# Kernel tuning notes

Hardware: AMD Instinct MI355X
Metric: run time of the kernel (lower is better)

Reference implementation:

```python
import math
import jax, jax.numpy as jnp
import numpy as np


def _sinkhorn_attn(q, n):
    """Log-domain Sinkhorn-Knopp, eps=1, max_iter=1, uniform marginals.
    cost C = -q @ q^T, so M = (-C + u + v)/eps = S + u + v with S = q q^T.
    Returns transport plan pi = exp(S + u_i + v_j).  q: [B, n, d]."""
    S = jnp.einsum('bnd,bmd->bnm', q, q)            # [B, n, n]
    log_marg = -math.log(n)                          # log(1/n)
    u = log_marg - jax.nn.logsumexp(S, axis=-1)      # [B, n] row update
    v = log_marg - jax.nn.logsumexp(S + u[..., :, None], axis=-2)  # [B, n] col update
    return jnp.exp(S + u[..., :, None] + v[..., None, :])


def reference(x, row_embed, col_embed):
    # x: [B, d, H, W]; row_embed/col_embed: [len_embedding, d//2]
    B, d, H, W = x.shape
    # learned positional embedding: [H, W, d] -> [d, H, W]
    x_emb = col_embed[:W]                             # [W, F]
    y_emb = row_embed[:H]                             # [H, F]
    F = x_emb.shape[-1]
    pos = jnp.concatenate([
        jnp.broadcast_to(x_emb[None, :, :], (H, W, F)),
        jnp.broadcast_to(y_emb[:, None, :], (H, W, F)),
    ], axis=-1).transpose(2, 0, 1)                    # [d, H, W]
    x = x + pos[None]

    n = H * W
    xf = x.reshape(B, d, n).transpose(0, 2, 1)        # [B, n, d] = q = k = v (v unscaled)
    inv_sqrtV = 1.0 / math.sqrt(math.sqrt(d))         # d**-0.25 applied to q and k each
    attn = _sinkhorn_attn(xf * inv_sqrtV, n)          # [B, n, n]
    out = jnp.einsum('bnm,bmd->bnd', attn, xf)        # [B, n, d]
    return out.transpose(0, 2, 1).reshape(B, d, H, W)


def setup_inputs() -> dict:
    key = jax.random.key(0)
    k1, k2, k3 = jax.random.split(key, 3)
    B, d, H, W = 32, 512, 32, 32
    len_emb, F = 32, d // 2
    return {
        'x': jax.random.normal(k1, (B, d, H, W), dtype=jnp.float32),
        'row_embed': jax.random.uniform(k2, (len_emb, F), dtype=jnp.float32),
        'col_embed': jax.random.uniform(k3, (len_emb, F), dtype=jnp.float32),
    }
```

## Files before the change

### kernel.cpp

```cpp
#include <hip/hip_runtime.h>
#include <hip/hip_fp16.h>
#include <math.h>

typedef _Float16 f16;
typedef _Float16 f16x8 __attribute__((ext_vector_type(8)));
typedef _Float16 f16x4 __attribute__((ext_vector_type(4)));
typedef float f32x4 __attribute__((ext_vector_type(4)));

namespace {
constexpr int kB = 32, kD = 512, kN = 1024, kF = 256;
constexpr float kScale = 0.04419417382415922f;
constexpr float kLogMarg = -6.931471805599453f;
constexpr float kMarg = 1.f / 1024.f;
constexpr float kPScale = 16384.f;
constexpr float kPInv = 1.f / 16384.f;
}

__device__ __forceinline__ void gload16(const void* g, void* l) {
  __builtin_amdgcn_global_load_lds(
      (const __attribute__((address_space(1))) void*)g,
      (__attribute__((address_space(3))) void*)l, 16, 0, 0);
}

__global__ __launch_bounds__(256) void k_prep(
    const float* __restrict__ x, const float* __restrict__ re,
    const float* __restrict__ ce, f16* __restrict__ xf,
    f16* __restrict__ xfT, int b0) {
  __shared__ f16 T[64][68];
  const int lb = blockIdx.z;
  const int i0 = blockIdx.x * 64, c0 = blockIdx.y * 64;
  const int t = threadIdx.x;
  const int il = (t & 15) * 4;
  const int cl = t >> 4;
  const size_t xbase = ((size_t)(b0 + lb) * kD) * kN;
#pragma unroll
  for (int p = 0; p < 4; p++) {
    const int c = c0 + cl + 16 * p;
    const int i = i0 + il;
    const float4 xv = *(const float4*)(x + xbase + (size_t)c * kN + i);
    float4 pv;
    if (c < kF) {
      pv.x = ce[((i + 0) & 31) * kF + c];
      pv.y = ce[((i + 1) & 31) * kF + c];
      pv.z = ce[((i + 2) & 31) * kF + c];
      pv.w = ce[((i + 3) & 31) * kF + c];
    } else {
      const float r = re[(i >> 5) * kF + (c - kF)];
      pv.x = r; pv.y = r; pv.z = r; pv.w = r;
    }
    const f16 h0 = (f16)(xv.x + pv.x), h1 = (f16)(xv.y + pv.y);
    const f16 h2 = (f16)(xv.z + pv.z), h3 = (f16)(xv.w + pv.w);
    f16* dT = xfT + ((size_t)lb * kD + c) * kN + i;
    *(f16x4*)dT = (f16x4){h0, h1, h2, h3};
    T[cl + 16 * p][il + 0] = h0; T[cl + 16 * p][il + 1] = h1;
    T[cl + 16 * p][il + 2] = h2; T[cl + 16 * p][il + 3] = h3;
  }
  __syncthreads();
#pragma unroll
  for (int p = 0; p < 4; p++) {
    const int ir = cl + 16 * p;
    const int cc = il;
    const f16 h0 = T[cc + 0][ir], h1 = T[cc + 1][ir];
    const f16 h2 = T[cc + 2][ir], h3 = T[cc + 3][ir];
    f16* dF = xf + ((size_t)lb * kN + i0 + ir) * kD + c0 + cc;
    *(f16x4*)dF = (f16x4){h0, h1, h2, h3};
  }
}

__global__ __launch_bounds__(512) void k_gemm_s(
    const f16* __restrict__ xf, f16* __restrict__ S16,
    float* __restrict__ rp) {
  __shared__ char sm[131072];
  const int nwg = (int)(gridDim.x * gridDim.y * gridDim.z);
  const int lin = (int)(blockIdx.x +
                        gridDim.x * (blockIdx.y + gridDim.y * blockIdx.z));
  const int wid = (lin & 7) * (nwg >> 3) + (lin >> 3);
  const int bx = wid & 3, by = (wid >> 2) & 3, bz = wid >> 4;

  const int lb = bz;
  const int i0 = by * 256, j0 = bx * 256;
  const char* base = (const char*)(xf + (size_t)lb * kN * kD);
  const int t = threadIdx.x;
  const int w = t >> 6, lane = t & 63;
  const int wm = w >> 2, wn = w & 3;
  const int m_off = wm * 128, n_off = wn * 64;
  const int quad = lane >> 4, l15 = lane & 15;
  const int swz = (l15 & 7) << 4;

  int srcA[4], srcB[4], ldsw[4];
#pragma unroll
  for (int p = 0; p < 4; p++) {
    const int off = p * 8192 + t * 16;
    const int r = off >> 7;
    const int cb = (off & 127) ^ ((r & 7) << 4);
    srcA[p] = (i0 + r) * (kD * 2) + cb;
    srcB[p] = (j0 + r) * (kD * 2) + cb;
    ldsw[p] = p * 8192 + w * 1024;
  }

  f32x4 acc[8][4];
#pragma unroll
  for (int a = 0; a < 8; a++)
#pragma unroll
    for (int b = 0; b < 4; b++) acc[a][b] = (f32x4){0.f, 0.f, 0.f, 0.f};

#pragma unroll
  for (int p = 0; p < 4; p++) gload16(base + srcA[p], sm + ldsw[p]);
#pragma unroll
  for (int p = 0; p < 4; p++) gload16(base + srcB[p], sm + 32768 + ldsw[p]);
  __syncthreads();

#pragma unroll
  for (int tt = 0; tt < 8; tt++) {
    const int cur = tt & 1, nxt = cur ^ 1;
    if (tt + 1 < 8) {
      const int k0b = (tt + 1) * 128;
#pragma unroll
      for (int p = 0; p < 4; p++)
        gload16(base + srcA[p] + k0b, sm + (nxt << 16) + ldsw[p]);
#pragma unroll
      for (int p = 0; p < 4; p++)
        gload16(base + srcB[p] + k0b, sm + (nxt << 16) + 32768 + ldsw[p]);
    }
    const char* bA = sm + (cur << 16);
    const char* bB = bA + 32768;
#pragma unroll
    for (int kk = 0; kk < 2; kk++) {
      f16x8 af[8], bf[4];
#pragma unroll
      for (int q = 0; q < 8; q++)
        af[q] = *(const f16x8*)(bA + (m_off + 16 * q + l15) * 128 +
                                ((kk * 64 + quad * 16) ^ swz));
#pragma unroll
      for (int q = 0; q < 4; q++)
        bf[q] = *(const f16x8*)(bB + (n_off + 16 * q + l15) * 128 +
                                ((kk * 64 + quad * 16) ^ swz));
#pragma unroll
      for (int qa = 0; qa < 8; qa++)
#pragma unroll
        for (int qb = 0; qb < 4; qb++)
          acc[qa][qb] = __builtin_amdgcn_mfma_f32_16x16x32_f16(
              af[qa], bf[qb], acc[qa][qb], 0, 0, 0);
    }
    __syncthreads();
  }

  f16* Sb = S16 + (size_t)lb * kN * kN;
  const int jt = bx * 4 + wn;
  float* rpb = rp + ((size_t)lb * 16 + jt) * kN + i0 + m_off;
#pragma unroll
  for (int qa = 0; qa < 8; qa++) {
    const int i = i0 + m_off + 16 * qa + quad * 4;
    float rs[4] = {0.f, 0.f, 0.f, 0.f};
#pragma unroll
    for (int qb = 0; qb < 4; qb++) {
      const int j = j0 + n_off + 16 * qb + l15;
#pragma unroll
      for (int r = 0; r < 4; r++) {
        const f16 h = (f16)(acc[qa][qb][r] * kScale);
        Sb[(size_t)(i + r) * kN + j] = h;
        rs[r] += __expf((float)h);
      }
    }
#pragma unroll
    for (int r = 0; r < 4; r++) {
      float s = rs[r];
      s += __shfl_xor(s, 1);
      s += __shfl_xor(s, 2);
      s += __shfl_xor(s, 4);
      s += __shfl_xor(s, 8);
      if (l15 == 0) rpb[16 * qa + 4 * quad + r] = s;
    }
  }
}

__global__ __launch_bounds__(256) void k_u(
    const float* __restrict__ rp, float* __restrict__ u) {
  const int lb = blockIdx.y;
  const int i = blockIdx.x * 256 + threadIdx.x;
  const float* r = rp + (size_t)lb * 16 * kN + i;
  float s = 0.f;
#pragma unroll
  for (int t = 0; t < 16; t++) s += r[(size_t)t * kN];
  u[lb * kN + i] = kLogMarg - __logf(s);
}

__global__ __launch_bounds__(256) void k_cs(
    const f16* __restrict__ S16, const float* __restrict__ u,
    float* __restrict__ cp, f16* __restrict__ E16) {
  const int lb = blockIdx.z;
  const int seg = blockIdx.y;
  const int j = blockIdx.x * 256 + threadIdx.x;
  const f16* Sb = S16 + (size_t)lb * kN * kN + j;
  f16* Eb = E16 + (size_t)lb * kN * kN + j;
  const float* ub = u + lb * kN + seg * 64;
  const size_t rbase = (size_t)(seg * 64) * kN;
  float s = 0.f;
#pragma unroll 4
  for (int r = 0; r < 64; r++) {
    const float eS = __expf((float)Sb[rbase + (size_t)r * kN] + ub[r]);
    s += eS;
    Eb[rbase + (size_t)r * kN] = (f16)(eS * kPScale);
  }
  cp[((size_t)lb * 16 + seg) * kN + j] = s;
}

__global__ __launch_bounds__(256) void k_v(
    const float* __restrict__ cp, float* __restrict__ ev) {
  const int lb = blockIdx.y;
  const int j = blockIdx.x * 256 + threadIdx.x;
  const float* c = cp + (size_t)lb * 16 * kN + j;
  float s = 0.f;
#pragma unroll
  for (int r = 0; r < 16; r++) s += c[(size_t)r * kN];
  ev[lb * kN + j] = kMarg / s;
}

__global__ __launch_bounds__(512) void k_gemm_o(
    const f16* __restrict__ xfT, const f16* __restrict__ E16,
    const float* __restrict__ ev, float* __restrict__ out, int b0) {
  __shared__ char sm[131072];
  const int nwg = (int)(gridDim.x * gridDim.y * gridDim.z);
  const int lin = (int)(blockIdx.x +
                        gridDim.x * (blockIdx.y + gridDim.y * blockIdx.z));
  const int wid = (lin & 7) * (nwg >> 3) + (lin >> 3);
  const int bx = wid & 3, by = (wid >> 2) & 1, bz = wid >> 3;

  const int lb = bz;
  const int i0 = bx * 256, c0 = by * 256;
  const char* Ab = (const char*)(xfT + (size_t)lb * kD * kN);
  const char* Bb = (const char*)(E16 + (size_t)lb * kN * kN);
  const float* evb = ev + (size_t)lb * kN;
  const int t = threadIdx.x;
  const int w = t >> 6, lane = t & 63;
  const int wm = w >> 2, wn = w & 3;
  const int m_off = wm * 128, n_off = wn * 64;
  const int quad = lane >> 4, l15 = lane & 15;
  const int swz = (l15 & 7) << 4;

  int srcAlin[4], dstA[4], srcB[4], ldsw[4], evcol[4];
#pragma unroll
  for (int p = 0; p < 4; p++) {
    const int off = p * 8192 + t * 16;
    const int r = off >> 7;
    const int cbl = off & 127;
    const int cb = cbl ^ ((r & 7) << 4);
    srcAlin[p] = (c0 + r) * (kN * 2) + cbl;
    dstA[p] = r * 128 + cb;
    srcB[p] = (i0 + r) * (kN * 2) + cb;
    ldsw[p] = p * 8192 + w * 1024;
    evcol[p] = cbl >> 1;
  }

  f32x4 acc[8][4];
#pragma unroll
  for (int a = 0; a < 8; a++)
#pragma unroll
    for (int b = 0; b < 4; b++) acc[a][b] = (f32x4){0.f, 0.f, 0.f, 0.f};

  f16x8 al[4];
  float4 e0[4], e1[4];
#pragma unroll
  for (int p = 0; p < 4; p++) {
    al[p] = *(const f16x8*)(Ab + srcAlin[p]);
    e0[p] = *(const float4*)(evb + evcol[p]);
    e1[p] = *(const float4*)(evb + evcol[p] + 4);
  }
#pragma unroll
  for (int p = 0; p < 4; p++) gload16(Bb + srcB[p], sm + 32768 + ldsw[p]);
#pragma unroll
  for (int p = 0; p < 4; p++) {
    f16x8 pr;
    pr[0] = (f16)((float)al[p][0] * e0[p].x);
    pr[1] = (f16)((float)al[p][1] * e0[p].y);
    pr[2] = (f16)((float)al[p][2] * e0[p].z);
    pr[3] = (f16)((float)al[p][3] * e0[p].w);
    pr[4] = (f16)((float)al[p][4] * e1[p].x);
    pr[5] = (f16)((float)al[p][5] * e1[p].y);
    pr[6] = (f16)((float)al[p][6] * e1[p].z);
    pr[7] = (f16)((float)al[p][7] * e1[p].w);
    *(f16x8*)(sm + dstA[p]) = pr;
  }
  __syncthreads();

#pragma unroll
  for (int tt = 0; tt < 16; tt++) {
    const int cur = tt & 1, nxt = cur ^ 1;
    const bool pf = (tt + 1 < 16);
    if (pf) {
      const int k0b = (tt + 1) * 128;
      const int k0f = (tt + 1) * 64;
#pragma unroll
      for (int p = 0; p < 4; p++) {
        al[p] = *(const f16x8*)(Ab + srcAlin[p] + k0b);
        e0[p] = *(const float4*)(evb + k0f + evcol[p]);
        e1[p] = *(const float4*)(evb + k0f + evcol[p] + 4);
      }
#pragma unroll
      for (int p = 0; p < 4; p++)
        gload16(Bb + srcB[p] + k0b, sm + (nxt << 16) + 32768 + ldsw[p]);
    }
    const char* bA = sm + (cur << 16);
    const char* bB = bA + 32768;
#pragma unroll
    for (int kk = 0; kk < 2; kk++) {
      f16x8 af[8], bf[4];
#pragma unroll
      for (int q = 0; q < 8; q++)
        af[q] = *(const f16x8*)(bA + (m_off + 16 * q + l15) * 128 +
                                ((kk * 64 + quad * 16) ^ swz));
#pragma unroll
      for (int q = 0; q < 4; q++)
        bf[q] = *(const f16x8*)(bB + (n_off + 16 * q + l15) * 128 +
                                ((kk * 64 + quad * 16) ^ swz));
#pragma unroll
      for (int qa = 0; qa < 8; qa++)
#pragma unroll
        for (int qb = 0; qb < 4; qb++)
          acc[qa][qb] = __builtin_amdgcn_mfma_f32_16x16x32_f16(
              af[qa], bf[qb], acc[qa][qb], 0, 0, 0);
    }
    if (pf) {
#pragma unroll
      for (int p = 0; p < 4; p++) {
        f16x8 pr;
        pr[0] = (f16)((float)al[p][0] * e0[p].x);
        pr[1] = (f16)((float)al[p][1] * e0[p].y);
        pr[2] = (f16)((float)al[p][2] * e0[p].z);
        pr[3] = (f16)((float)al[p][3] * e0[p].w);
        pr[4] = (f16)((float)al[p][4] * e1[p].x);
        pr[5] = (f16)((float)al[p][5] * e1[p].y);
        pr[6] = (f16)((float)al[p][6] * e1[p].z);
        pr[7] = (f16)((float)al[p][7] * e1[p].w);
        *(f16x8*)(sm + (nxt << 16) + dstA[p]) = pr;
      }
    }
    __syncthreads();
  }

  float* ob = out + ((size_t)(b0 + lb) * kD) * kN;
#pragma unroll
  for (int qa = 0; qa < 8; qa++) {
    const int c = c0 + m_off + 16 * qa + quad * 4;
#pragma unroll
    for (int qb = 0; qb < 4; qb++) {
      const int i = i0 + n_off + 16 * qb + l15;
#pragma unroll
      for (int r = 0; r < 4; r++)
        ob[(size_t)(c + r) * kN + i] = acc[qa][qb][r] * kPInv;
    }
  }
}

extern "C" void kernel_launch(void* const* d_in, const int* in_sizes, int n_in,
                              void* d_out, int out_size, void* d_ws, size_t ws_size,
                              hipStream_t stream) {
  const float* x = (const float*)d_in[0];
  const float* re = (const float*)d_in[1];
  const float* ce = (const float*)d_in[2];
  float* out = (float*)d_out;

  char* wsb = (char*)d_ws;
  const size_t perb = 2097152ull + 1048576 + 1048576 + 2097152 +
                      4096 + 4096 + 65536 + 65536;
  int G = (int)(ws_size / perb);
  if (G >= 32) G = 32;
  else if (G >= 16) G = 16;
  else if (G >= 8) G = 8;
  else if (G >= 4) G = 4;
  else if (G < 1) G = 1;
  f16* S16 = (f16*)wsb;
  f16* xf = (f16*)(wsb + (size_t)G * 2097152);
  f16* xfT = (f16*)((char*)xf + (size_t)G * 1048576);
  f16* E16 = (f16*)((char*)xfT + (size_t)G * 1048576);
  float* u = (float*)((char*)E16 + (size_t)G * 2097152);
  float* ev = u + (size_t)G * kN;
  float* rp = ev + (size_t)G * kN;
  float* cp = rp + (size_t)G * 16 * kN;

  for (int b0 = 0; b0 < kB; b0 += G) {
    const int g = (kB - b0 < G) ? (kB - b0) : G;
    k_prep<<<dim3(16, 8, g), 256, 0, stream>>>(x, re, ce, xf, xfT, b0);
    k_gemm_s<<<dim3(4, 4, g), 512, 0, stream>>>(xf, S16, rp);
    k_u<<<dim3(4, g), 256, 0, stream>>>(rp, u);
    k_cs<<<dim3(4, 16, g), 256, 0, stream>>>(S16, u, cp, E16);
    k_v<<<dim3(4, g), 256, 0, stream>>>(cp, ev);
    k_gemm_o<<<dim3(4, 2, g), 512, 0, stream>>>(xfT, E16, ev, out, b0);
  }
}
```

Baseline: 257.0 us.

## Interleave async LDS loads with MFMA in both GEMMs; prescale V in separate kernel

Both GEMM main loops are restructured so the next tile's global-to-LDS loads are issued in pieces between MFMA groups. Explicit vmcnt waits, raw s_barrier calls and s_setprio replace __syncthreads, and the A fragments are loaded per sub-block to reduce register pressure. The ev column scaling of V, previously done in registers inside k_gemm_o, moves into a new k_va kernel that writes a scaled f16 copy aT, so the output GEMM can use direct async LDS loads for both operands. This costs an extra 1 MB per batch of workspace plus one extra read and write pass over xfT.

```diff
diff --git a/kernel.cpp b/kernel.cpp
--- a/kernel.cpp
+++ b/kernel.cpp
@@ -98,51 +98,69 @@
     ldsw[p] = p * 8192 + w * 1024;
   }
 
+#pragma unroll
+  for (int p = 0; p < 4; p++) gload16(base + srcA[p], sm + ldsw[p]);
+#pragma unroll
+  for (int p = 0; p < 4; p++) gload16(base + srcB[p], sm + 32768 + ldsw[p]);
+
   f32x4 acc[8][4];
 #pragma unroll
   for (int a = 0; a < 8; a++)
 #pragma unroll
     for (int b = 0; b < 4; b++) acc[a][b] = (f32x4){0.f, 0.f, 0.f, 0.f};
-
-#pragma unroll
-  for (int p = 0; p < 4; p++) gload16(base + srcA[p], sm + ldsw[p]);
-#pragma unroll
-  for (int p = 0; p < 4; p++) gload16(base + srcB[p], sm + 32768 + ldsw[p]);
-  __syncthreads();
 
 #pragma unroll
   for (int tt = 0; tt < 8; tt++) {
     const int cur = tt & 1, nxt = cur ^ 1;
-    if (tt + 1 < 8) {
-      const int k0b = (tt + 1) * 128;
-#pragma unroll
-      for (int p = 0; p < 4; p++)
-        gload16(base + srcA[p] + k0b, sm + (nxt << 16) + ldsw[p]);
-#pragma unroll
-      for (int p = 0; p < 4; p++)
-        gload16(base + srcB[p] + k0b, sm + (nxt << 16) + 32768 + ldsw[p]);
-    }
-    const char* bA = sm + (cur << 16);
-    const char* bB = bA + 32768;
-#pragma unroll
-    for (int kk = 0; kk < 2; kk++) {
-      f16x8 af[8], bf[4];
-#pragma unroll
-      for (int q = 0; q < 8; q++)
-        af[q] = *(const f16x8*)(bA + (m_off + 16 * q + l15) * 128 +
-                                ((kk * 64 + quad * 16) ^ swz));
-#pragma unroll
-      for (int q = 0; q < 4; q++)
-        bf[q] = *(const f16x8*)(bB + (n_off + 16 * q + l15) * 128 +
-                                ((kk * 64 + quad * 16) ^ swz));
-#pragma unroll
-      for (int qa = 0; qa < 8; qa++)
+    const char* rA = sm + (cur << 16);
+    const char* rB = rA + 32768;
+    char* wA = sm + (nxt << 16);
+    char* wB = wA + 32768;
+    const int k0b = (tt + 1) * 128;
+    f16x8 bf[4][2];
+#pragma unroll
+    for (int q = 0; q < 4; q++) {
+      if (q == 0) {
+        if (tt + 1 < 8) {
+          gload16(base + srcA[0] + k0b, wA + ldsw[0]);
+          gload16(base + srcB[0] + k0b, wB + ldsw[0]);
+          asm volatile("s_waitcnt vmcnt(2)" ::: "memory");
+        } else {
+          asm volatile("s_waitcnt vmcnt(0)" ::: "memory");
+        }
+        __builtin_amdgcn_s_barrier();
 #pragma unroll
         for (int qb = 0; qb < 4; qb++)
-          acc[qa][qb] = __builtin_amdgcn_mfma_f32_16x16x32_f16(
-              af[qa], bf[qb], acc[qa][qb], 0, 0, 0);
-    }
-    __syncthreads();
+#pragma unroll
+          for (int kk = 0; kk < 2; kk++)
+            bf[qb][kk] = *(const f16x8*)(rB + (n_off + 16 * qb + l15) * 128 +
+                                         ((kk * 64 + quad * 16) ^ swz));
+      } else {
+        if (tt + 1 < 8) {
+          gload16(base + srcA[q] + k0b, wA + ldsw[q]);
+          gload16(base + srcB[q] + k0b, wB + ldsw[q]);
+        }
+      }
+      f16x8 af[2][2];
+#pragma unroll
+      for (int pa = 0; pa < 2; pa++)
+#pragma unroll
+        for (int kk = 0; kk < 2; kk++)
+          af[pa][kk] = *(const f16x8*)(rA + (m_off + 16 * (2 * q + pa) + l15) * 128 +
+                                       ((kk * 64 + quad * 16) ^ swz));
+      __builtin_amdgcn_s_barrier();
+      __builtin_amdgcn_s_setprio(1);
+#pragma unroll
+      for (int pa = 0; pa < 2; pa++)
+#pragma unroll
+        for (int qb = 0; qb < 4; qb++)
+#pragma unroll
+          for (int kk = 0; kk < 2; kk++)
+            acc[2 * q + pa][qb] = __builtin_amdgcn_mfma_f32_16x16x32_f16(
+                af[pa][kk], bf[qb][kk], acc[2 * q + pa][qb], 0, 0, 0);
+      __builtin_amdgcn_s_setprio(0);
+    }
+    __builtin_amdgcn_s_barrier();
   }
 
   f16* Sb = S16 + (size_t)lb * kN * kN;
@@ -205,20 +223,27 @@
   cp[((size_t)lb * 16 + seg) * kN + j] = s;
 }
 
-__global__ __launch_bounds__(256) void k_v(
-    const float* __restrict__ cp, float* __restrict__ ev) {
-  const int lb = blockIdx.y;
+__global__ __launch_bounds__(256) void k_va(
+    const float* __restrict__ cp, const f16* __restrict__ xfT,
+    f16* __restrict__ aT) {
+  const int lb = blockIdx.z;
   const int j = blockIdx.x * 256 + threadIdx.x;
-  const float* c = cp + (size_t)lb * 16 * kN + j;
+  const int c0 = blockIdx.y * 128;
+  const float* cpb = cp + (size_t)lb * 16 * kN + j;
   float s = 0.f;
 #pragma unroll
-  for (int r = 0; r < 16; r++) s += c[(size_t)r * kN];
-  ev[lb * kN + j] = kMarg / s;
+  for (int r = 0; r < 16; r++) s += cpb[(size_t)r * kN];
+  const float evj = kMarg / s;
+  const f16* src = xfT + (size_t)lb * kD * kN + (size_t)c0 * kN + j;
+  f16* dst = aT + (size_t)lb * kD * kN + (size_t)c0 * kN + j;
+#pragma unroll 8
+  for (int c = 0; c < 128; c++)
+    dst[(size_t)c * kN] = (f16)((float)src[(size_t)c * kN] * evj);
 }
 
 __global__ __launch_bounds__(512) void k_gemm_o(
-    const f16* __restrict__ xfT, const f16* __restrict__ E16,
-    const float* __restrict__ ev, float* __restrict__ out, int b0) {
+    const f16* __restrict__ aT, const f16* __restrict__ E16,
+    float* __restrict__ out, int b0) {
   __shared__ char sm[131072];
   const int nwg = (int)(gridDim.x * gridDim.y * gridDim.z);
   const int lin = (int)(blockIdx.x +
@@ -228,9 +253,8 @@
 
   const int lb = bz;
   const int i0 = bx * 256, c0 = by * 256;
-  const char* Ab = (const char*)(xfT + (size_t)lb * kD * kN);
+  const char* Ab = (const char*)(aT + (size_t)lb * kD * kN);
   const char* Bb = (const char*)(E16 + (size_t)lb * kN * kN);
-  const float* evb = ev + (size_t)lb * kN;
   const int t = threadIdx.x;
   const int w = t >> 6, lane = t & 63;
   const int wm = w >> 2, wn = w & 3;
@@ -238,104 +262,80 @@
   const int quad = lane >> 4, l15 = lane & 15;
   const int swz = (l15 & 7) << 4;
 
-  int srcAlin[4], dstA[4], srcB[4], ldsw[4], evcol[4];
+  int srcA[4], srcB[4], ldsw[4];
 #pragma unroll
   for (int p = 0; p < 4; p++) {
     const int off = p * 8192 + t * 16;
     const int r = off >> 7;
-    const int cbl = off & 127;
-    const int cb = cbl ^ ((r & 7) << 4);
-    srcAlin[p] = (c0 + r) * (kN * 2) + cbl;
-    dstA[p] = r * 128 + cb;
+    const int cb = (off & 127) ^ ((r & 7) << 4);
+    srcA[p] = (c0 + r) * (kN * 2) + cb;
     srcB[p] = (i0 + r) * (kN * 2) + cb;
     ldsw[p] = p * 8192 + w * 1024;
-    evcol[p] = cbl >> 1;
-  }
+  }
+
+#pragma unroll
+  for (int p = 0; p < 4; p++) gload16(Ab + srcA[p], sm + ldsw[p]);
+#pragma unroll
+  for (int p = 0; p < 4; p++) gload16(Bb + srcB[p], sm + 32768 + ldsw[p]);
 
   f32x4 acc[8][4];
 #pragma unroll
   for (int a = 0; a < 8; a++)
 #pragma unroll
     for (int b = 0; b < 4; b++) acc[a][b] = (f32x4){0.f, 0.f, 0.f, 0.f};
-
-  f16x8 al[4];
-  float4 e0[4], e1[4];
-#pragma unroll
-  for (int p = 0; p < 4; p++) {
-    al[p] = *(const f16x8*)(Ab + srcAlin[p]);
-    e0[p] = *(const float4*)(evb + evcol[p]);
-    e1[p] = *(const float4*)(evb + evcol[p] + 4);
-  }
-#pragma unroll
-  for (int p = 0; p < 4; p++) gload16(Bb + srcB[p], sm + 32768 + ldsw[p]);
-#pragma unroll
-  for (int p = 0; p < 4; p++) {
-    f16x8 pr;
-    pr[0] = (f16)((float)al[p][0] * e0[p].x);
-    pr[1] = (f16)((float)al[p][1] * e0[p].y);
-    pr[2] = (f16)((float)al[p][2] * e0[p].z);
-    pr[3] = (f16)((float)al[p][3] * e0[p].w);
-    pr[4] = (f16)((float)al[p][4] * e1[p].x);
-    pr[5] = (f16)((float)al[p][5] * e1[p].y);
-    pr[6] = (f16)((float)al[p][6] * e1[p].z);
-    pr[7] = (f16)((float)al[p][7] * e1[p].w);
-    *(f16x8*)(sm + dstA[p]) = pr;
-  }
-  __syncthreads();
 
 #pragma unroll
   for (int tt = 0; tt < 16; tt++) {
     const int cur = tt & 1, nxt = cur ^ 1;
-    const bool pf = (tt + 1 < 16);
-    if (pf) {
-      const int k0b = (tt + 1) * 128;
-      const int k0f = (tt + 1) * 64;
-#pragma unroll
-      for (int p = 0; p < 4; p++) {
-        al[p] = *(const f16x8*)(Ab + srcAlin[p] + k0b);
-        e0[p] = *(const float4*)(evb + k0f + evcol[p]);
-        e1[p] = *(const float4*)(evb + k0f + evcol[p] + 4);
+    const char* rA = sm + (cur << 16);
+    const char* rB = rA + 32768;
+    char* wA = sm + (nxt << 16);
+    char* wB = wA + 32768;
+    const int k0b = (tt + 1) * 128;
+    f16x8 bf[4][2];
+#pragma unroll
+    for (int q = 0; q < 4; q++) {
+      if (q == 0) {
+        if (tt + 1 < 16) {
+          gload16(Ab + srcA[0] + k0b, wA + ldsw[0]);
+          gload16(Bb + srcB[0] + k0b, wB + ldsw[0]);
+          asm volatile("s_waitcnt vmcnt(2)" ::: "memory");
+        } else {
+          asm volatile("s_waitcnt vmcnt(0)" ::: "memory");
+        }
+        __builtin_amdgcn_s_barrier();
+#pragma unroll
+        for (int qb = 0; qb < 4; qb++)
+#pragma unroll
+          for (int kk = 0; kk < 2; kk++)
+            bf[qb][kk] = *(const f16x8*)(rB + (n_off + 16 * qb + l15) * 128 +
+                                         ((kk * 64 + quad * 16) ^ swz));
+      } else {
+        if (tt + 1 < 16) {
+          gload16(Ab + srcA[q] + k0b, wA + ldsw[q]);
+          gload16(Bb + srcB[q] + k0b, wB + ldsw[q]);
+        }
       }
-#pragma unroll
-      for (int p = 0; p < 4; p++)
-        gload16(Bb + srcB[p] + k0b, sm + (nxt << 16) + 32768 + ldsw[p]);
-    }
-    const char* bA = sm + (cur << 16);
-    const char* bB = bA + 32768;
-#pragma unroll
-    for (int kk = 0; kk < 2; kk++) {
-      f16x8 af[8], bf[4];
-#pragma unroll
-      for (int q = 0; q < 8; q++)
-        af[q] = *(const f16x8*)(bA + (m_off + 16 * q + l15) * 128 +
-                                ((kk * 64 + quad * 16) ^ swz));
-#pragma unroll
-      for (int q = 0; q < 4; q++)
-        bf[q] = *(const f16x8*)(bB + (n_off + 16 * q + l15) * 128 +
-                                ((kk * 64 + quad * 16) ^ swz));
-#pragma unroll
-      for (int qa = 0; qa < 8; qa++)
+      f16x8 af[2][2];
+#pragma unroll
+      for (int pa = 0; pa < 2; pa++)
+#pragma unroll
+        for (int kk = 0; kk < 2; kk++)
+          af[pa][kk] = *(const f16x8*)(rA + (m_off + 16 * (2 * q + pa) + l15) * 128 +
+                                       ((kk * 64 + quad * 16) ^ swz));
+      __builtin_amdgcn_s_barrier();
+      __builtin_amdgcn_s_setprio(1);
+#pragma unroll
+      for (int pa = 0; pa < 2; pa++)
 #pragma unroll
         for (int qb = 0; qb < 4; qb++)
-          acc[qa][qb] = __builtin_amdgcn_mfma_f32_16x16x32_f16(
-              af[qa], bf[qb], acc[qa][qb], 0, 0, 0);
-    }
-    if (pf) {
-#pragma unroll
-      for (int p = 0; p < 4; p++) {
-        f16x8 pr;
-        pr[0] = (f16)((float)al[p][0] * e0[p].x);
-        pr[1] = (f16)((float)al[p][1] * e0[p].y);
-        pr[2] = (f16)((float)al[p][2] * e0[p].z);
-        pr[3] = (f16)((float)al[p][3] * e0[p].w);
-        pr[4] = (f16)((float)al[p][4] * e1[p].x);
-        pr[5] = (f16)((float)al[p][5] * e1[p].y);
-        pr[6] = (f16)((float)al[p][6] * e1[p].z);
-        pr[7] = (f16)((float)al[p][7] * e1[p].w);
-        *(f16x8*)(sm + (nxt << 16) + dstA[p]) = pr;
-      }
-    }
-    __syncthreads();
+#pragma unroll
+          for (int kk = 0; kk < 2; kk++)
+            acc[2 * q + pa][qb] = __builtin_amdgcn_mfma_f32_16x16x32_f16(
+                af[pa][kk], bf[qb][kk], acc[2 * q + pa][qb], 0, 0, 0);
+      __builtin_amdgcn_s_setprio(0);
+    }
+    __builtin_amdgcn_s_barrier();
   }
 
   float* ob = out + ((size_t)(b0 + lb) * kD) * kN;
@@ -361,8 +361,8 @@
   float* out = (float*)d_out;
 
   char* wsb = (char*)d_ws;
-  const size_t perb = 2097152ull + 1048576 + 1048576 + 2097152 +
-                      4096 + 4096 + 65536 + 65536;
+  const size_t perb = 2097152ull + 1048576 + 1048576 + 2097152 + 1048576 +
+                      4096 + 65536 + 65536;
   int G = (int)(ws_size / perb);
   if (G >= 32) G = 32;
   else if (G >= 16) G = 16;
@@ -373,9 +373,9 @@
   f16* xf = (f16*)(wsb + (size_t)G * 2097152);
   f16* xfT = (f16*)((char*)xf + (size_t)G * 1048576);
   f16* E16 = (f16*)((char*)xfT + (size_t)G * 1048576);
-  float* u = (float*)((char*)E16 + (size_t)G * 2097152);
-  float* ev = u + (size_t)G * kN;
-  float* rp = ev + (size_t)G * kN;
+  f16* aT = (f16*)((char*)E16 + (size_t)G * 2097152);
+  float* u = (float*)((char*)aT + (size_t)G * 1048576);
+  float* rp = u + (size_t)G * kN;
   float* cp = rp + (size_t)G * 16 * kN;
 
   for (int b0 = 0; b0 < kB; b0 += G) {
@@ -384,7 +384,7 @@
     k_gemm_s<<<dim3(4, 4, g), 512, 0, stream>>>(xf, S16, rp);
     k_u<<<dim3(4, g), 256, 0, stream>>>(rp, u);
     k_cs<<<dim3(4, 16, g), 256, 0, stream>>>(S16, u, cp, E16);
-    k_v<<<dim3(4, g), 256, 0, stream>>>(cp, ev);
-    k_gemm_o<<<dim3(4, 2, g), 512, 0, stream>>>(xfT, E16, ev, out, b0);
-  }
-}
+    k_va<<<dim3(4, 4, g), 256, 0, stream>>>(cp, xfT, aT);
+    k_gemm_o<<<dim3(4, 2, g), 512, 0, stream>>>(aT, E16, out, b0);
+  }
+}
```

Result: faster. 245.4 us (-4.5%).
